# Optimization experiments

Hardware: AMD Instinct MI355X
Metric: run time of the kernel (lower is better)

The kernel has to match this reference:

```python
import jax, jax.numpy as jnp
import numpy as np

VOCAB = 50257
EMBED = 1024
MAX_CTX = 8192
SEQ = 8192


def setup_inputs() -> dict:
    key = jax.random.key(0)
    k1, k2, k3 = jax.random.split(key, 3)
    x = jax.random.randint(k1, (SEQ,), 0, VOCAB, dtype=jnp.int32)
    # Dense kernels: one_hot @ W + b  <=>  table lookup with rows of W
    W_tok = jax.random.normal(k2, (VOCAB, EMBED), dtype=jnp.float32) * 0.02
    b_tok = jnp.zeros((EMBED,), dtype=jnp.float32)
    W_pos = jax.random.normal(k3, (MAX_CTX, EMBED), dtype=jnp.float32) * 0.02
    b_pos = jnp.zeros((EMBED,), dtype=jnp.float32)
    return {"x": x, "W_tok": W_tok, "b_tok": b_tok, "W_pos": W_pos, "b_pos": b_pos}


def reference(x, W_tok, b_tok, W_pos, b_pos):
    # one_hot(x, V) @ W_tok + b_tok == W_tok[x] + b_tok (tokens are in-range)
    S = x.shape[0]
    pos = (S - 1) - jnp.arange(S)  # original uses reversed positions
    token_embedding = W_tok[x] + b_tok            # [S, D]
    position_embedding = W_pos[pos] + b_pos       # [S, D]
    return token_embedding + position_embedding  # [S, D]
```

## Files before the change

### kernel.cpp

```cpp
#include <hip/hip_runtime.h>

__global__ void __launch_bounds__(256)
embedding_kernel(const int* __restrict__ x,
                 const float4* __restrict__ W_tok,
                 const float4* __restrict__ b_tok,
                 const float4* __restrict__ W_pos,
                 const float4* __restrict__ b_pos,
                 float4* __restrict__ out,
                 int S) {
    const int s = blockIdx.x;
    const int d = threadIdx.x;
    const int tok = x[s];
    const int pos = (S - 1) - s;

    const float4 a  = W_tok[(size_t)tok * 256 + d];
    const float4 b  = W_pos[(size_t)pos * 256 + d];
    const float4 bt = b_tok[d];
    const float4 bp = b_pos[d];

    float4 r;
    r.x = a.x + b.x + bt.x + bp.x;
    r.y = a.y + b.y + bt.y + bp.y;
    r.z = a.z + b.z + bt.z + bp.z;
    r.w = a.w + b.w + bt.w + bp.w;

    out[(size_t)s * 256 + d] = r;
}

extern "C" void kernel_launch(void* const* d_in, const int* in_sizes, int n_in,
                              void* d_out, int out_size, void* d_ws, size_t ws_size,
                              hipStream_t stream) {
    const int*    x     = (const int*)   d_in[0];
    const float4* W_tok = (const float4*)d_in[1];
    const float4* b_tok = (const float4*)d_in[2];
    const float4* W_pos = (const float4*)d_in[3];
    const float4* b_pos = (const float4*)d_in[4];
    float4* out = (float4*)d_out;

    const int S = in_sizes[0];

    embedding_kernel<<<S, 256, 0, stream>>>(x, W_tok, b_tok, W_pos, b_pos, out, S);
}
```

Before: 278.3 us.

## Process eight rows per block with batched loads and nontemporal hints

Each block now handles eight sequence rows, issuing all token and position row loads before any arithmetic so more memory requests are in flight per thread. The bias sum is computed once per thread and reused across rows. Position-table loads and output stores use nontemporal hints to avoid polluting cache with streaming data. This cuts the block count by eight, which may reduce occupancy-driven latency hiding, and it assumes the sequence length is a multiple of eight.

```diff
diff --git a/kernel.cpp b/kernel.cpp
--- a/kernel.cpp
+++ b/kernel.cpp
@@ -1,43 +1,54 @@
 #include <hip/hip_runtime.h>
+
+typedef float v4f __attribute__((ext_vector_type(4)));
+
+#define ROWS_PER_BLOCK 8
 
 __global__ void __launch_bounds__(256)
 embedding_kernel(const int* __restrict__ x,
-                 const float4* __restrict__ W_tok,
-                 const float4* __restrict__ b_tok,
-                 const float4* __restrict__ W_pos,
-                 const float4* __restrict__ b_pos,
-                 float4* __restrict__ out,
+                 const v4f* __restrict__ W_tok,
+                 const v4f* __restrict__ b_tok,
+                 const v4f* __restrict__ W_pos,
+                 const v4f* __restrict__ b_pos,
+                 v4f* __restrict__ out,
                  int S) {
-    const int s = blockIdx.x;
     const int d = threadIdx.x;
-    const int tok = x[s];
-    const int pos = (S - 1) - s;
+    const int s0 = blockIdx.x * ROWS_PER_BLOCK;
 
-    const float4 a  = W_tok[(size_t)tok * 256 + d];
-    const float4 b  = W_pos[(size_t)pos * 256 + d];
-    const float4 bt = b_tok[d];
-    const float4 bp = b_pos[d];
+    const v4f bt = b_tok[d];
+    const v4f bp = b_pos[d];
+    const v4f bsum = bt + bp;
 
-    float4 r;
-    r.x = a.x + b.x + bt.x + bp.x;
-    r.y = a.y + b.y + bt.y + bp.y;
-    r.z = a.z + b.z + bt.z + bp.z;
-    r.w = a.w + b.w + bt.w + bp.w;
+    int tok[ROWS_PER_BLOCK];
+#pragma unroll
+    for (int r = 0; r < ROWS_PER_BLOCK; ++r) tok[r] = x[s0 + r];
 
-    out[(size_t)s * 256 + d] = r;
+    v4f a[ROWS_PER_BLOCK], p[ROWS_PER_BLOCK];
+#pragma unroll
+    for (int r = 0; r < ROWS_PER_BLOCK; ++r) {
+        a[r] = W_tok[(size_t)tok[r] * 256 + d];
+        p[r] = __builtin_nontemporal_load(&W_pos[(size_t)(S - 1 - (s0 + r)) * 256 + d]);
+    }
+
+#pragma unroll
+    for (int r = 0; r < ROWS_PER_BLOCK; ++r) {
+        v4f o = a[r] + p[r] + bsum;
+        __builtin_nontemporal_store(o, &out[(size_t)(s0 + r) * 256 + d]);
+    }
 }
 
 extern "C" void kernel_launch(void* const* d_in, const int* in_sizes, int n_in,
                               void* d_out, int out_size, void* d_ws, size_t ws_size,
                               hipStream_t stream) {
-    const int*    x     = (const int*)   d_in[0];
-    const float4* W_tok = (const float4*)d_in[1];
-    const float4* b_tok = (const float4*)d_in[2];
-    const float4* W_pos = (const float4*)d_in[3];
-    const float4* b_pos = (const float4*)d_in[4];
-    float4* out = (float4*)d_out;
+    const int* x     = (const int*)d_in[0];
+    const v4f* W_tok = (const v4f*)d_in[1];
+    const v4f* b_tok = (const v4f*)d_in[2];
+    const v4f* W_pos = (const v4f*)d_in[3];
+    const v4f* b_pos = (const v4f*)d_in[4];
+    v4f* out = (v4f*)d_out;
 
     const int S = in_sizes[0];
 
-    embedding_kernel<<<S, 256, 0, stream>>>(x, W_tok, b_tok, W_pos, b_pos, out, S);
+    embedding_kernel<<<S / ROWS_PER_BLOCK, 256, 0, stream>>>(
+        x, W_tok, b_tok, W_pos, b_pos, out, S);
 }
```

After: 276.8 us. About the same (-0.5%).
